# Performance work log

Hardware: AMD Instinct MI355X
Metric: run time of the kernel (lower is better)

The kernel has to match this reference:

```python
import jax, jax.numpy as jnp
import numpy as np

N_PAIRS = 64000
N_ATOMS = 16000
N_PAIR_FEATURES = 8
N_HIDDEN = 100


def setup_inputs() -> dict:
    key = jax.random.key(0)
    k1, k2, k3, k4 = jax.random.split(key, 4)
    pair_features = jax.random.normal(k1, (N_PAIRS, N_PAIR_FEATURES), dtype=jnp.float32)
    atom_features = jax.random.normal(k2, (N_ATOMS, N_HIDDEN), dtype=jnp.float32)
    atom_to_pair = jax.random.randint(k3, (N_PAIRS, 2), 0, N_ATOMS, dtype=jnp.int32)
    W = jax.random.normal(k4, (N_PAIR_FEATURES, N_HIDDEN * N_HIDDEN), dtype=jnp.float32) * 0.1
    b = jnp.zeros((N_HIDDEN * N_HIDDEN,), dtype=jnp.float32)
    return {"pair_features": pair_features, "atom_features": atom_features,
            "atom_to_pair": atom_to_pair, "W": W, "b": b}


def reference(pair_features, atom_features, atom_to_pair, W, b):
    n_atoms, n_hidden = atom_features.shape
    # Dense projection: [E, F] @ [F, H*H] -> per-edge HxH matrices
    A = (pair_features @ W + b).reshape(-1, n_hidden, n_hidden)  # [E, H, H]
    # Gather source-atom features (column 1 of atom_to_pair)
    src = atom_features[atom_to_pair[:, 1]]                      # [E, H]
    # Batched matrix-vector multiply per edge
    msg = jnp.einsum('eij,ej->ei', A, src)                       # [E, H]
    # Scatter-reduce messages onto destination atoms (column 0)
    return jax.ops.segment_sum(msg, atom_to_pair[:, 0], num_segments=n_atoms)
```

## Files before the change

### kernel.cpp

```cpp
#include <hip/hip_runtime.h>
#include <hip/hip_bf16.h>

#define N_PAIRS   64000
#define N_ATOMS   16000
#define N_FEAT    8
#define N_HIDDEN  100
#define SW        1024
#define SKL       936
#define MAX_DEG   64

#define N_SETUP   (112 * 1024)
#define SETUP_BLOCKS (N_SETUP / 256)
#define HIST_BLOCKS  (N_PAIRS / 256)

typedef __attribute__((ext_vector_type(8))) short bf16x8_t;
typedef __attribute__((ext_vector_type(4))) float f32x4_t;

__global__ __launch_bounds__(256) void setup_hist(const float* __restrict__ W,
                                                  const float* __restrict__ b,
                                                  const int* __restrict__ a2p,
                                                  const float* __restrict__ pf,
                                                  __hip_bfloat16* __restrict__ wtb2,
                                                  int* __restrict__ deg,
                                                  unsigned* __restrict__ bucket,
                                                  float* __restrict__ pfb) {
    int bid = blockIdx.x;
    if (bid < SETUP_BLOCKS) {
        int id = bid * 256 + threadIdx.x;
        int i = id >> 10;
        int k = id & 1023;
        float v = 0.f;
        if (i < N_HIDDEN) {
            if (k < 800) {
                int f = k / N_HIDDEN;
                int j = k - f * N_HIDDEN;
                v = W[f * (N_HIDDEN * N_HIDDEN) + i * N_HIDDEN + j];
            } else if (k < 900) {
                int j = k - 800;
                v = b[i * N_HIDDEN + j];
            }
        }
        wtb2[id] = __float2bfloat16(v);
    } else {
        int e = (bid - SETUP_BLOCKS) * 256 + threadIdx.x;
        int dest = a2p[e * 2];
        int src  = a2p[e * 2 + 1];
        int slot = atomicAdd(&deg[dest], 1);
        if (slot < MAX_DEG) {
            bucket[dest * MAX_DEG + slot] = (unsigned)src;
            const float4* ps = (const float4*)(pf + e * N_FEAT);
            float4* pd = (float4*)(pfb + ((size_t)dest * MAX_DEG + slot) * N_FEAT);
            pd[0] = ps[0];
            pd[1] = ps[1];
        }
    }
}

__global__ __launch_bounds__(512) void fused_edge_gemm(const float* __restrict__ af,
                                                       const int* __restrict__ deg,
                                                       const unsigned* __restrict__ bucket,
                                                       const float* __restrict__ pfb,
                                                       const __hip_bfloat16* __restrict__ wtb2,
                                                       float* __restrict__ out) {
    __shared__ __hip_bfloat16 St[16 * SKL];
    int blk  = blockIdx.x;
    int wave = threadIdx.x >> 6;
    int lane = threadIdx.x & 63;
    int h    = lane >> 5;
    int l    = lane & 31;
    int r    = wave * 2 + h;
    int d    = blk * 16 + r;
    bool act = (l < 25);

    int n = deg[d];
    if (n > 32) n = 32;

    unsigned src_l = 0;
    if (l < n) src_l = bucket[d * MAX_DEG + l];

    const float* pfb_d = pfb + (size_t)d * MAX_DEG * N_FEAT;
    float acc[9][4] = {};

    for (int t0 = 0; t0 < n; t0 += 4) {
        int s = t0 + (l >> 3);
        float pfv = (s < n) ? pfb_d[s * N_FEAT + (l & 7)] : 0.f;
        float4 a[4];
#pragma unroll
        for (int u = 0; u < 4; ++u) {
            int t = t0 + u;
            int src = __shfl((int)src_l, h * 32 + (t < n ? t : 0), 64);
            if (t < n && act)
                a[u] = *(const float4*)(af + src * N_HIDDEN + 4 * l);
            else
                a[u] = make_float4(0.f, 0.f, 0.f, 0.f);
        }
#pragma unroll
        for (int u = 0; u < 4; ++u) {
            float av0 = a[u].x, av1 = a[u].y, av2 = a[u].z, av3 = a[u].w;
#pragma unroll
            for (int f = 0; f < N_FEAT; ++f) {
                float p = __shfl(pfv, h * 32 + u * 8 + f, 64);
                acc[f][0] += p * av0;
                acc[f][1] += p * av1;
                acc[f][2] += p * av2;
                acc[f][3] += p * av3;
            }
            acc[8][0] += av0;
            acc[8][1] += av1;
            acc[8][2] += av2;
            acc[8][3] += av3;
        }
    }

    __hip_bfloat16* srow = St + r * SKL;
    if (act) {
#pragma unroll
        for (int f = 0; f < 9; ++f) {
            __hip_bfloat162 h0, h1;
            h0.x = __float2bfloat16(acc[f][0]);
            h0.y = __float2bfloat16(acc[f][1]);
            h1.x = __float2bfloat16(acc[f][2]);
            h1.y = __float2bfloat16(acc[f][3]);
            *(__hip_bfloat162*)(srow + f * N_HIDDEN + 4 * l)     = h0;
            *(__hip_bfloat162*)(srow + f * N_HIDDEN + 4 * l + 2) = h1;
        }
    } else {
        __hip_bfloat162 z;
        z.x = __float2bfloat16(0.f);
        z.y = z.x;
        *(__hip_bfloat162*)(srow + 900 + 4 * (l - 25))     = z;
        *(__hip_bfloat162*)(srow + 900 + 4 * (l - 25) + 2) = z;
    }
    __syncthreads();

    if (wave < 7) {
        int quad = lane >> 4;
        int l15  = lane & 15;
        int m0   = blk * 16;
        const __hip_bfloat16* as = St + l15 * SKL + quad * 8;
        const __hip_bfloat16* bp = wtb2 + (size_t)(wave * 16 + l15) * SW + quad * 8;
        f32x4_t accd = {0.f, 0.f, 0.f, 0.f};
#pragma unroll
        for (int k = 0; k < 29; ++k) {
            bf16x8_t aa = *(const bf16x8_t*)(as + k * 32);
            bf16x8_t bb = *(const bf16x8_t*)(bp + k * 32);
            accd = __builtin_amdgcn_mfma_f32_16x16x32_bf16(aa, bb, accd, 0, 0, 0);
        }
        int c = wave * 16 + l15;
        if (c < N_HIDDEN) {
#pragma unroll
            for (int rr = 0; rr < 4; ++rr)
                out[(size_t)(m0 + quad * 4 + rr) * N_HIDDEN + c] = accd[rr];
        }
    }
}

extern "C" void kernel_launch(void* const* d_in, const int* in_sizes, int n_in,
                              void* d_out, int out_size, void* d_ws, size_t ws_size,
                              hipStream_t stream) {
    const float* pf  = (const float*)d_in[0];
    const float* af  = (const float*)d_in[1];
    const int*   a2p = (const int*)d_in[2];
    const float* W   = (const float*)d_in[3];
    const float* b   = (const float*)d_in[4];
    float* out = (float*)d_out;

    char* ws = (char*)d_ws;
    __hip_bfloat16* wtb2 = (__hip_bfloat16*)ws;
    int* deg             = (int*)(ws + 229376);
    unsigned* bucket     = (unsigned*)(ws + 229376 + 64000);
    float* pfb           = (float*)(ws + 229376 + 64000 + 4096000);

    hipMemsetAsync(deg, 0, N_ATOMS * sizeof(int), stream);
    setup_hist<<<SETUP_BLOCKS + HIST_BLOCKS, 256, 0, stream>>>(W, b, a2p, pf, wtb2, deg, bucket, pfb);
    fused_edge_gemm<<<N_ATOMS / 16, 512, 0, stream>>>(af, deg, bucket, pfb, wtb2, out);
}
```

Measured before the change: 111.1 us.

## Gather bf16 atom features, shrink blocks to 8 rows, unroll edge loop by 8

Setup now converts atom_features to a padded bf16 copy, so the per-edge gather in the fused kernel reads half the bytes. The edge loop handles 8 neighbours per iteration to put more loads in flight. Blocks shrink to 256 threads and 8 destination atoms, with waves looping over the 7 MFMA column tiles. Half of each 16-row MFMA tile is now duplicate rows that are computed and thrown away, and rounding the gathered features to bf16 adds error.

Result: slower. 136.9 us (+23.3%).

```diff
diff --git a/kernel.cpp b/kernel.cpp
--- a/kernel.cpp
+++ b/kernel.cpp
@@ -7,10 +7,12 @@
 #define N_HIDDEN  100
 #define SW        1024
 #define SKL       936
+#define SAF       104
 #define MAX_DEG   64
 
-#define N_SETUP   (112 * 1024)
-#define SETUP_BLOCKS (N_SETUP / 256)
+#define AFB_ELEMS   (N_ATOMS * SAF)
+#define AFB_BLOCKS  ((AFB_ELEMS + 255) / 256)
+#define SETUP_BLOCKS (112 * 1024 / 256)
 #define HIST_BLOCKS  (N_PAIRS / 256)
 
 typedef __attribute__((ext_vector_type(8))) short bf16x8_t;
@@ -20,13 +22,23 @@
                                                   const float* __restrict__ b,
                                                   const int* __restrict__ a2p,
                                                   const float* __restrict__ pf,
+                                                  const float* __restrict__ af,
                                                   __hip_bfloat16* __restrict__ wtb2,
+                                                  __hip_bfloat16* __restrict__ afb,
                                                   int* __restrict__ deg,
                                                   unsigned* __restrict__ bucket,
                                                   float* __restrict__ pfb) {
     int bid = blockIdx.x;
-    if (bid < SETUP_BLOCKS) {
+    if (bid < AFB_BLOCKS) {
         int id = bid * 256 + threadIdx.x;
+        if (id < AFB_ELEMS) {
+            int row = id / SAF;
+            int k   = id - row * SAF;
+            float v = (k < N_HIDDEN) ? af[row * N_HIDDEN + k] : 0.f;
+            afb[id] = __float2bfloat16(v);
+        }
+    } else if (bid < AFB_BLOCKS + SETUP_BLOCKS) {
+        int id = (bid - AFB_BLOCKS) * 256 + threadIdx.x;
         int i = id >> 10;
         int k = id & 1023;
         float v = 0.f;
@@ -42,7 +54,7 @@
         }
         wtb2[id] = __float2bfloat16(v);
     } else {
-        int e = (bid - SETUP_BLOCKS) * 256 + threadIdx.x;
+        int e = (bid - AFB_BLOCKS - SETUP_BLOCKS) * 256 + threadIdx.x;
         int dest = a2p[e * 2];
         int src  = a2p[e * 2 + 1];
         int slot = atomicAdd(&deg[dest], 1);
@@ -56,20 +68,20 @@
     }
 }
 
-__global__ __launch_bounds__(512) void fused_edge_gemm(const float* __restrict__ af,
+__global__ __launch_bounds__(256) void fused_edge_gemm(const __hip_bfloat16* __restrict__ afb,
                                                        const int* __restrict__ deg,
                                                        const unsigned* __restrict__ bucket,
                                                        const float* __restrict__ pfb,
                                                        const __hip_bfloat16* __restrict__ wtb2,
                                                        float* __restrict__ out) {
-    __shared__ __hip_bfloat16 St[16 * SKL];
+    __shared__ __hip_bfloat16 St[8 * SKL];
     int blk  = blockIdx.x;
     int wave = threadIdx.x >> 6;
     int lane = threadIdx.x & 63;
     int h    = lane >> 5;
     int l    = lane & 31;
     int r    = wave * 2 + h;
-    int d    = blk * 16 + r;
+    int d    = blk * 8 + r;
     bool act = (l < 25);
 
     int n = deg[d];
@@ -81,25 +93,31 @@
     const float* pfb_d = pfb + (size_t)d * MAX_DEG * N_FEAT;
     float acc[9][4] = {};
 
-    for (int t0 = 0; t0 < n; t0 += 4) {
-        int s = t0 + (l >> 3);
-        float pfv = (s < n) ? pfb_d[s * N_FEAT + (l & 7)] : 0.f;
-        float4 a[4];
+    for (int t0 = 0; t0 < n; t0 += 8) {
+        int s0 = t0 + (l >> 3);
+        int s1 = s0 + 4;
+        float pfv0 = (s0 < n) ? pfb_d[s0 * N_FEAT + (l & 7)] : 0.f;
+        float pfv1 = (s1 < n) ? pfb_d[s1 * N_FEAT + (l & 7)] : 0.f;
+        ushort4 a[8];
 #pragma unroll
-        for (int u = 0; u < 4; ++u) {
+        for (int u = 0; u < 8; ++u) {
             int t = t0 + u;
             int src = __shfl((int)src_l, h * 32 + (t < n ? t : 0), 64);
             if (t < n && act)
-                a[u] = *(const float4*)(af + src * N_HIDDEN + 4 * l);
+                a[u] = *(const ushort4*)(afb + src * SAF + 4 * l);
             else
-                a[u] = make_float4(0.f, 0.f, 0.f, 0.f);
+                a[u] = make_ushort4(0, 0, 0, 0);
         }
 #pragma unroll
-        for (int u = 0; u < 4; ++u) {
-            float av0 = a[u].x, av1 = a[u].y, av2 = a[u].z, av3 = a[u].w;
+        for (int u = 0; u < 8; ++u) {
+            float av0 = __uint_as_float((unsigned)a[u].x << 16);
+            float av1 = __uint_as_float((unsigned)a[u].y << 16);
+            float av2 = __uint_as_float((unsigned)a[u].z << 16);
+            float av3 = __uint_as_float((unsigned)a[u].w << 16);
+            float pfsrc = (u < 4) ? pfv0 : pfv1;
 #pragma unroll
             for (int f = 0; f < N_FEAT; ++f) {
-                float p = __shfl(pfv, h * 32 + u * 8 + f, 64);
+                float p = __shfl(pfsrc, h * 32 + (u & 3) * 8 + f, 64);
                 acc[f][0] += p * av0;
                 acc[f][1] += p * av1;
                 acc[f][2] += p * av2;
@@ -133,12 +151,12 @@
     }
     __syncthreads();
 
-    if (wave < 7) {
-        int quad = lane >> 4;
-        int l15  = lane & 15;
-        int m0   = blk * 16;
-        const __hip_bfloat16* as = St + l15 * SKL + quad * 8;
-        const __hip_bfloat16* bp = wtb2 + (size_t)(wave * 16 + l15) * SW + quad * 8;
+    int quad = lane >> 4;
+    int l15  = lane & 15;
+    int m0   = blk * 8;
+    const __hip_bfloat16* as = St + (l15 & 7) * SKL + quad * 8;
+    for (int nt = wave; nt < 7; nt += 4) {
+        const __hip_bfloat16* bp = wtb2 + (size_t)(nt * 16 + l15) * SW + quad * 8;
         f32x4_t accd = {0.f, 0.f, 0.f, 0.f};
 #pragma unroll
         for (int k = 0; k < 29; ++k) {
@@ -146,8 +164,8 @@
             bf16x8_t bb = *(const bf16x8_t*)(bp + k * 32);
             accd = __builtin_amdgcn_mfma_f32_16x16x32_bf16(aa, bb, accd, 0, 0, 0);
         }
-        int c = wave * 16 + l15;
-        if (c < N_HIDDEN) {
+        int c = nt * 16 + l15;
+        if (quad < 2 && c < N_HIDDEN) {
 #pragma unroll
             for (int rr = 0; rr < 4; ++rr)
                 out[(size_t)(m0 + quad * 4 + rr) * N_HIDDEN + c] = accd[rr];
@@ -170,8 +188,10 @@
     int* deg             = (int*)(ws + 229376);
     unsigned* bucket     = (unsigned*)(ws + 229376 + 64000);
     float* pfb           = (float*)(ws + 229376 + 64000 + 4096000);
+    __hip_bfloat16* afb  = (__hip_bfloat16*)(ws + 229376 + 64000 + 4096000 + 32768000);
 
     hipMemsetAsync(deg, 0, N_ATOMS * sizeof(int), stream);
-    setup_hist<<<SETUP_BLOCKS + HIST_BLOCKS, 256, 0, stream>>>(W, b, a2p, pf, wtb2, deg, bucket, pfb);
-    fused_edge_gemm<<<N_ATOMS / 16, 512, 0, stream>>>(af, deg, bucket, pfb, wtb2, out);
+    setup_hist<<<AFB_BLOCKS + SETUP_BLOCKS + HIST_BLOCKS, 256, 0, stream>>>(
+        W, b, a2p, pf, af, wtb2, afb, deg, bucket, pfb);
+    fused_edge_gemm<<<N_ATOMS / 8, 256, 0, stream>>>(afb, deg, bucket, pfb, wtb2, out);
 }
```
